# Optimization experiments

Hardware: AMD Instinct MI355X
Metric: run time of the kernel (lower is better)

The kernel has to match this reference:

```python
import jax, jax.numpy as jnp
import numpy as np

B, S, D, H = 4, 2048, 512, 8
DH = D // H


def setup_inputs() -> dict:
    key = jax.random.key(0)
    ks = jax.random.split(key, 6)
    embeddings = jax.random.normal(ks[0], (B, S, D), dtype=jnp.float32)
    token_masks = jax.random.randint(ks[1], (B, S), 0, 2, dtype=jnp.int32)
    # keras 'random_normal' initializer: stddev 0.05
    Wq = 0.05 * jax.random.normal(ks[2], (D, D), dtype=jnp.float32)
    Wk = 0.05 * jax.random.normal(ks[3], (D, D), dtype=jnp.float32)
    Wv = 0.05 * jax.random.normal(ks[4], (D, D), dtype=jnp.float32)
    Wo = 0.05 * jax.random.normal(ks[5], (D, D), dtype=jnp.float32)
    return {"embeddings": embeddings, "token_masks": token_masks,
            "Wq": Wq, "Wk": Wk, "Wv": Wv, "Wo": Wo}


def reference(embeddings, token_masks, Wq, Wk, Wv, Wo):
    b, s, d = embeddings.shape
    h, dh = H, d // H
    # QKV projections -> (b, h, s, dh)
    def split_heads(x):
        return x.reshape(b, s, h, dh).transpose(0, 2, 1, 3)
    Q = split_heads(embeddings @ Wq)
    K = split_heads(embeddings @ Wk)
    V = split_heads(embeddings @ Wv)
    scores = jnp.einsum('bhqd,bhkd->bhqk', Q, K) / jnp.sqrt(jnp.float32(dh))
    # causal (lower-triangular) mask combined with padding mask on both q and k
    causal = jnp.tril(jnp.ones((s, s), dtype=jnp.float32))
    tm = token_masks.astype(jnp.float32)
    attn_mask = causal[None, None, :, :] * tm[:, None, None, :] * tm[:, None, :, None]
    scores = jnp.where(attn_mask > 0, scores, jnp.float32(-1e30))
    weights = jax.nn.softmax(scores, axis=-1)  # dropout omitted (inference/eval mode)
    context = jnp.einsum('bhqk,bhkd->bhqd', weights, V)
    context = context.transpose(0, 2, 1, 3).reshape(b, s, d)
    return context @ Wo
```

## Files before the change

kernel.cpp:

```cpp
#include <hip/hip_runtime.h>
#include <hip/hip_bf16.h>
#include <stdint.h>

#define BATCH 4
#define SEQ 2048
#define DMODEL 512
#define NHEAD 8
#define HD 64

#define C1 0.18033688f
#define BIAS2 -23.0831207f

using f32x4 = __attribute__((ext_vector_type(4))) float;
using bfrag = __attribute__((ext_vector_type(8))) short;

__device__ __forceinline__ short f2bf(float f) {
  uint32_t x = __builtin_bit_cast(uint32_t, f);
  uint32_t r = (x + 0x7fffu + ((x >> 16) & 1u)) >> 16;
  return (short)r;
}
__device__ __forceinline__ short f2bf_fast(float f) {
  return (short)((__builtin_bit_cast(uint32_t, f) + 0x8000u) >> 16);
}
__device__ __forceinline__ float bf2f(short s) {
  return __builtin_bit_cast(float, ((uint32_t)(uint16_t)s) << 16);
}
__device__ __forceinline__ void gl_lds16(const void* g, void* l) {
  __builtin_amdgcn_global_load_lds(
      (const __attribute__((address_space(1))) void*)g,
      (__attribute__((address_space(3))) void*)l, 16, 0, 0);
}
__device__ __forceinline__ bool sniff_f32(const void* p, int tid) {
  const uint32_t* xw = (const uint32_t*)p;
  const int lane = tid & 63;
  const uint32_t w1 = xw[lane], w2 = xw[64 + lane];
  bool bad = (((w1 >> 7) & 0xffu) >= 0xB0u) | (((w1 >> 23) & 0xffu) >= 0xB0u) |
             (((w2 >> 7) & 0xffu) >= 0xB0u) | (((w2 >> 23) & 0xffu) >= 0xB0u);
  return __ballot(bad) != 0ull;
}

__global__ __launch_bounds__(256) void prep(const void* __restrict__ X,
                                            const void* __restrict__ w0,
                                            const void* __restrict__ w1,
                                            const void* __restrict__ w2,
                                            const void* __restrict__ w3,
                                            short* __restrict__ Xb,
                                            short* __restrict__ wtAll,
                                            float* __restrict__ mv) {
  const int blk = blockIdx.x, tid = threadIdx.x;
  if (blk < 2048) {
    const bool isf32 = sniff_f32(X, tid);
    const int i = (blk * 256 + tid) * 8;
    if (isf32) {
      const float* f = (const float*)X;
      short r[8];
#pragma unroll
      for (int j = 0; j < 8; ++j) r[j] = f2bf(f[i + j]);
      *(bfrag*)&Xb[i] = *(bfrag*)r;
    } else {
      *(bfrag*)&Xb[i] = *(const bfrag*)&((const short*)X)[i];
    }
  } else if (blk < 3072) {
    __shared__ short t[32][33];
    const int idx = blk - 2048;
    const int z = idx >> 8, rem = idx & 255;
    const void* in = (z == 0) ? w0 : (z == 1) ? w1 : (z == 2) ? w2 : w3;
    short* out = wtAll + (size_t)z * DMODEL * DMODEL;
    const int tx = tid & 31, ty = tid >> 5;
    const bool isf32 = sniff_f32(in, tid);
    const int n0 = (rem & 15) * 32, k0 = (rem >> 4) * 32;
#pragma unroll
    for (int i = ty; i < 32; i += 8) {
      const int idx2 = (k0 + i) * DMODEL + n0 + tx;
      t[i][tx] = isf32 ? f2bf(((const float*)in)[idx2]) : ((const short*)in)[idx2];
    }
    __syncthreads();
#pragma unroll
    for (int i = ty; i < 32; i += 8) out[(n0 + i) * DMODEL + k0 + tx] = t[tx][i];
  } else {
#pragma unroll
    for (int j = 0; j < 8; ++j) mv[tid * 8 + j] = 0.f;
  }
}

__global__ __launch_bounds__(256) void gemm_qkv(const short* __restrict__ X,
                                                const short* __restrict__ WtAll,
                                                short* __restrict__ Qo,
                                                short* __restrict__ Ko,
                                                short* __restrict__ Vo,
                                                float* __restrict__ mv) {
  __shared__ __align__(16) short As[2][128 * 32];
  __shared__ __align__(16) short Bs[2][128 * 32];
  const int which = blockIdx.z;
  const short* Wt = WtAll + which * DMODEL * DMODEL;
  const int m0 = blockIdx.y * 128, n0 = blockIdx.x * 128;
  const int tid = threadIdx.x, lane = tid & 63, wave = tid >> 6;
  const int l15 = lane & 15, quad = lane >> 4;
  const int wm = wave >> 1, wn = wave & 1;
  const int lrow = lane >> 2, lcol = (lane & 3) * 8;
  f32x4 acc[4][4] = {};
  auto stage = [&](int kc, int bb) {
#pragma unroll
    for (int i = 0; i < 2; ++i) {
      const int r0 = (wave * 2 + i) * 16;
      gl_lds16(&X[(size_t)(m0 + r0 + lrow) * DMODEL + kc + lcol], &As[bb][r0 * 32]);
      gl_lds16(&Wt[(size_t)(n0 + r0 + lrow) * DMODEL + kc + lcol], &Bs[bb][r0 * 32]);
    }
  };
  stage(0, 0);
  __syncthreads();
  int bb = 0;
  for (int kc = 0; kc < DMODEL; kc += 32) {
    if (kc + 32 < DMODEL) stage(kc + 32, bb ^ 1);
    bfrag a[4], b[4];
#pragma unroll
    for (int t = 0; t < 4; ++t) {
      a[t] = *(const bfrag*)&As[bb][(wm * 64 + t * 16 + l15) * 32 + quad * 8];
      b[t] = *(const bfrag*)&Bs[bb][(wn * 64 + t * 16 + l15) * 32 + quad * 8];
    }
#pragma unroll
    for (int tm = 0; tm < 4; ++tm)
#pragma unroll
      for (int tn = 0; tn < 4; ++tn)
        acc[tm][tn] = __builtin_amdgcn_mfma_f32_16x16x32_bf16(a[tm], b[tn], acc[tm][tn], 0, 0, 0);
    __syncthreads();
    bb ^= 1;
  }
  short* O = (which == 0) ? Qo : (which == 1) ? Ko : Vo;
#pragma unroll
  for (int tn = 0; tn < 4; ++tn) {
    const int col = n0 + wn * 64 + tn * 16 + l15;
    const int h = col >> 6, d = col & 63;
#pragma unroll
    for (int tm = 0; tm < 4; ++tm) {
#pragma unroll
      for (int r = 0; r < 4; ++r) {
        const int row = m0 + wm * 64 + tm * 16 + quad * 4 + r;
        const int b = row >> 11, s = row & 2047;
        O[((b * NHEAD + h) * SEQ + s) * HD + d] = f2bf(acc[tm][tn][r]);
      }
    }
  }
  if (which == 2) {
    const int b = (m0 + wm * 64) >> 11;
#pragma unroll
    for (int tn = 0; tn < 4; ++tn) {
      float s = 0.f;
#pragma unroll
      for (int tm = 0; tm < 4; ++tm)
#pragma unroll
        for (int r = 0; r < 4; ++r) s += acc[tm][tn][r];
      s += __shfl_xor(s, 16);
      s += __shfl_xor(s, 32);
      if (quad == 0) {
        const int col = n0 + wn * 64 + tn * 16 + l15;
        const int h = col >> 6, d = col & 63;
        atomicAdd(&mv[(b * NHEAD + h) * 64 + d], s);
      }
    }
  }
}

__global__ __launch_bounds__(256) void gemm_out(const short* __restrict__ X,
                                                const short* __restrict__ Wt,
                                                float* __restrict__ O) {
  __shared__ __align__(16) short As[2][128 * 32];
  __shared__ __align__(16) short Bs[2][128 * 32];
  const int m0 = blockIdx.y * 128, n0 = blockIdx.x * 128;
  const int tid = threadIdx.x, lane = tid & 63, wave = tid >> 6;
  const int l15 = lane & 15, quad = lane >> 4;
  const int wm = wave >> 1, wn = wave & 1;
  const int lrow = lane >> 2, lcol = (lane & 3) * 8;
  f32x4 acc[4][4] = {};
  auto stage = [&](int kc, int bb) {
#pragma unroll
    for (int i = 0; i < 2; ++i) {
      const int r0 = (wave * 2 + i) * 16;
      gl_lds16(&X[(size_t)(m0 + r0 + lrow) * DMODEL + kc + lcol], &As[bb][r0 * 32]);
      gl_lds16(&Wt[(size_t)(n0 + r0 + lrow) * DMODEL + kc + lcol], &Bs[bb][r0 * 32]);
    }
  };
  stage(0, 0);
  __syncthreads();
  int bb = 0;
  for (int kc = 0; kc < DMODEL; kc += 32) {
    if (kc + 32 < DMODEL) stage(kc + 32, bb ^ 1);
    bfrag a[4], b[4];
#pragma unroll
    for (int t = 0; t < 4; ++t) {
      a[t] = *(const bfrag*)&As[bb][(wm * 64 + t * 16 + l15) * 32 + quad * 8];
      b[t] = *(const bfrag*)&Bs[bb][(wn * 64 + t * 16 + l15) * 32 + quad * 8];
    }
#pragma unroll
    for (int tm = 0; tm < 4; ++tm)
#pragma unroll
      for (int tn = 0; tn < 4; ++tn)
        acc[tm][tn] = __builtin_amdgcn_mfma_f32_16x16x32_bf16(a[tm], b[tn], acc[tm][tn], 0, 0, 0);
    __syncthreads();
    bb ^= 1;
  }
#pragma unroll
  for (int tm = 0; tm < 4; ++tm)
#pragma unroll
    for (int tn = 0; tn < 4; ++tn) {
      const int col = n0 + wn * 64 + tn * 16 + l15;
#pragma unroll
      for (int r = 0; r < 4; ++r) {
        const int row = m0 + wm * 64 + tm * 16 + quad * 4 + r;
        O[(size_t)row * DMODEL + col] = acc[tm][tn][r];
      }
    }
}

__global__ __launch_bounds__(256, 4) void attn(const short* __restrict__ Q,
                                               const short* __restrict__ K,
                                               const short* __restrict__ V,
                                               const int* __restrict__ tmask,
                                               const float* __restrict__ meanV,
                                               short* __restrict__ ctx) {
  __shared__ __align__(16) short Ks[64 * 72];
  __shared__ __align__(16) short Vts[64 * 64];
  __shared__ __align__(16) short Ps[4 * 16 * 64];
  __shared__ int tmq[64];
  __shared__ int tmk[64];
  const int m2 = blockIdx.x >> 3, a3 = blockIdx.x & 7;
  const int j2 = blockIdx.y >> 3, b3 = blockIdx.y & 7;
  const int quart = (m2 + j2) & 3;
  const int qi = quart * 8 + ((quart & 1) ? (7 - a3) : a3);
  const int bh = j2 * 8 + b3;
  const int b = bh >> 3, h = bh & 7;
  const int q0 = qi * 64;
  const int tid = threadIdx.x, lane = tid & 63, wave = tid >> 6;
  const int l15 = lane & 15, quad = lane >> 4;
  const size_t base = (size_t)bh * SEQ * HD;

  bfrag qa0 = *(const bfrag*)&Q[base + (size_t)(q0 + wave * 16 + l15) * HD + quad * 8];
  bfrag qa1 = *(const bfrag*)&Q[base + (size_t)(q0 + wave * 16 + l15) * HD + 32 + quad * 8];
  if (tid < 64) tmq[tid] = tmask[b * SEQ + q0 + tid];

  f32x4 accO[4] = {};
  float lrow[4] = {0.f, 0.f, 0.f, 0.f};

  const int rp = tid >> 3, sgp = tid & 7;
  bfrag kA, kB, vA, vB;
  int tmreg = 0;

  auto prefetch = [&](int kc) {
    const size_t o0 = base + (size_t)(kc + 2 * rp) * HD + sgp * 8;
    kA = *(const bfrag*)&K[o0];
    kB = *(const bfrag*)&K[o0 + HD];
    vA = *(const bfrag*)&V[o0];
    vB = *(const bfrag*)&V[o0 + HD];
    if (tid < 64) tmreg = tmask[b * SEQ + kc + tid];
  };
  auto store_lds = [&]() {
    *(bfrag*)&Ks[(2 * rp) * 72 + sgp * 8] = kA;
    *(bfrag*)&Ks[(2 * rp + 1) * 72 + sgp * 8] = kB;
    const int g = ((rp >> 2) ^ ((sgp & 1) << 2) ^ (sgp >> 1)) & 7;
    const int kpos = (2 * rp) & 7;
#pragma unroll
    for (int j = 0; j < 8; ++j) {
      const uint32_t w = (uint32_t)(uint16_t)vA[j] | ((uint32_t)(uint16_t)vB[j] << 16);
      *(uint32_t*)&Vts[(sgp * 8 + j) * 64 + g * 8 + kpos] = w;
    }
    if (tid < 64) tmk[tid] = tmreg;
  };
  auto compute = [&](bool diag) {
    f32x4 sacc[4] = {};
#pragma unroll
    for (int t = 0; t < 4; ++t) {
      bfrag b0 = *(const bfrag*)&Ks[(t * 16 + l15) * 72 + quad * 8];
      sacc[t] = __builtin_amdgcn_mfma_f32_16x16x32_bf16(qa0, b0, sacc[t], 0, 0, 0);
    }
#pragma unroll
    for (int t = 0; t < 4; ++t) {
      bfrag b1 = *(const bfrag*)&Ks[(t * 16 + l15) * 72 + 32 + quad * 8];
      sacc[t] = __builtin_amdgcn_mfma_f32_16x16x32_bf16(qa1, b1, sacc[t], 0, 0, 0);
    }
    float badd[4];
#pragma unroll
    for (int t = 0; t < 4; ++t) badd[t] = tmk[t * 16 + l15] ? BIAS2 : -1e30f;
#pragma unroll
    for (int r = 0; r < 4; ++r) {
      const int m = quad * 4 + r;
#pragma unroll
      for (int t = 0; t < 4; ++t) {
        float p = exp2f(fmaf(sacc[t][r], C1, badd[t]));
        if (diag && (t * 16 + l15 > wave * 16 + m)) p = 0.f;
        lrow[r] += p;
        const int g = ((t * 2 + (l15 >> 3)) ^ (m & 7) ^ ((m >> 3) << 1)) & 7;
        Ps[wave * 1024 + m * 64 + g * 8 + (l15 & 7)] = f2bf_fast(p);
      }
    }
#pragma unroll
    for (int ks = 0; ks < 2; ++ks) {
#pragma unroll
      for (int t = 0; t < 4; ++t) {
        const int gp = ((ks * 4 + quad) ^ (l15 & 7) ^ ((l15 >> 3) << 1)) & 7;
        bfrag pa = *(const bfrag*)&Ps[wave * 1024 + l15 * 64 + gp * 8];
        const int d = t * 16 + l15;
        const int gv = ((ks * 4 + quad) ^ ((l15 >> 3) << 2) ^ t) & 7;
        bfrag vb = *(const bfrag*)&Vts[d * 64 + gv * 8];
        accO[t] = __builtin_amdgcn_mfma_f32_16x16x32_bf16(pa, vb, accO[t], 0, 0, 0);
      }
    }
  };

  prefetch(0);
  for (int kc = 0; kc <= q0; kc += 64) {
    __syncthreads();
    store_lds();
    __syncthreads();
    if (kc < q0) prefetch(kc + 64);
    compute(kc == q0);
  }

#pragma unroll
  for (int r = 0; r < 4; ++r) {
    float l = lrow[r];
    l += __shfl_xor(l, 1);
    l += __shfl_xor(l, 2);
    l += __shfl_xor(l, 4);
    l += __shfl_xor(l, 8);
    lrow[r] = 1.f / l;
  }
  const int qrow_loc = wave * 16 + quad * 4;
#pragma unroll
  for (int t = 0; t < 4; ++t) {
    const int d = t * 16 + l15;
    const float mvd = meanV[bh * 64 + d] * (1.f / 2048.f);
#pragma unroll
    for (int r = 0; r < 4; ++r) {
      const int row = qrow_loc + r;
      float val = accO[t][r] * lrow[r];
      if (tmq[row] == 0) val = mvd;
      ctx[((size_t)(b * SEQ + q0 + row)) * DMODEL + h * HD + d] = f2bf(val);
    }
  }
}

extern "C" void kernel_launch(void* const* d_in, const int* in_sizes, int n_in,
                              void* d_out, int out_size, void* d_ws, size_t ws_size,
                              hipStream_t stream) {
  const void* X = d_in[0];
  const int* tmask = (const int*)d_in[1];
  const void* Wq = d_in[2];
  const void* Wk = d_in[3];
  const void* Wv = d_in[4];
  const void* Wo = d_in[5];
  float* out = (float*)d_out;
  char* ws = (char*)d_ws;

  const size_t WELEM = (size_t)DMODEL * DMODEL;
  const size_t TELEM = (size_t)BATCH * NHEAD * SEQ * HD;

  float* mv = (float*)(ws + 4096);
  short* wt = (short*)(ws + 4096 + 8192);
  short* Xb = (short*)(ws + 4096 + 8192 + 2097152);
  short* Qb = Xb + TELEM;
  short* Kb = Qb + TELEM;
  short* Vb = Kb + TELEM;
  short* Cb = Vb + TELEM;

  prep<<<3073, 256, 0, stream>>>(X, Wq, Wk, Wv, Wo, Xb, wt, mv);
  gemm_qkv<<<dim3(4, 64, 3), 256, 0, stream>>>(Xb, wt, Qb, Kb, Vb, mv);
  attn<<<dim3(32, 32), 256, 0, stream>>>(Qb, Kb, Vb, tmask, mv, Cb);
  gemm_out<<<dim3(4, 64), 256, 0, stream>>>(Cb, wt + 3 * WELEM, out);
}
```

Measured before the change: 163.9 us.

## Use two waves per attention block, each handling 32 query rows

The attention block shrinks from four to two waves, and each wave now processes two 16-row query tiles. Every K and V fragment read from LDS therefore feeds two MFMAs, and the cooperative K/V load covers four rows per thread instead of two. This raises register pressure and halves the threads per block, which could lower latency hiding and occupancy. The launch bounds are changed to match.

Result: slower. 228.8 us (+39.6%).

```diff
diff --git a/kernel.cpp b/kernel.cpp
--- a/kernel.cpp
+++ b/kernel.cpp
@@ -212,7 +212,7 @@
     }
 }
 
-__global__ __launch_bounds__(256, 4) void attn(const short* __restrict__ Q,
+__global__ __launch_bounds__(128, 3) void attn(const short* __restrict__ Q,
                                                const short* __restrict__ K,
                                                const short* __restrict__ V,
                                                const int* __restrict__ tmask,
@@ -220,7 +220,7 @@
                                                short* __restrict__ ctx) {
   __shared__ __align__(16) short Ks[64 * 72];
   __shared__ __align__(16) short Vts[64 * 64];
-  __shared__ __align__(16) short Ps[4 * 16 * 64];
+  __shared__ __align__(16) short Ps[2 * 32 * 64];
   __shared__ int tmq[64];
   __shared__ int tmk[64];
   const int m2 = blockIdx.x >> 3, a3 = blockIdx.x & 7;
@@ -234,48 +234,62 @@
   const int l15 = lane & 15, quad = lane >> 4;
   const size_t base = (size_t)bh * SEQ * HD;
 
-  bfrag qa0 = *(const bfrag*)&Q[base + (size_t)(q0 + wave * 16 + l15) * HD + quad * 8];
-  bfrag qa1 = *(const bfrag*)&Q[base + (size_t)(q0 + wave * 16 + l15) * HD + 32 + quad * 8];
+  const size_t qr0 = base + (size_t)(q0 + wave * 16 + l15) * HD;
+  const size_t qr1 = qr0 + (size_t)32 * HD;
+  bfrag q00 = *(const bfrag*)&Q[qr0 + quad * 8];
+  bfrag q01 = *(const bfrag*)&Q[qr0 + 32 + quad * 8];
+  bfrag q10 = *(const bfrag*)&Q[qr1 + quad * 8];
+  bfrag q11 = *(const bfrag*)&Q[qr1 + 32 + quad * 8];
   if (tid < 64) tmq[tid] = tmask[b * SEQ + q0 + tid];
 
-  f32x4 accO[4] = {};
-  float lrow[4] = {0.f, 0.f, 0.f, 0.f};
+  f32x4 accO0[4] = {}, accO1[4] = {};
+  float lr0[4] = {0.f, 0.f, 0.f, 0.f}, lr1[4] = {0.f, 0.f, 0.f, 0.f};
 
   const int rp = tid >> 3, sgp = tid & 7;
-  bfrag kA, kB, vA, vB;
+  bfrag kA, kB, kC, kD, vA, vB, vC, vD;
   int tmreg = 0;
 
   auto prefetch = [&](int kc) {
-    const size_t o0 = base + (size_t)(kc + 2 * rp) * HD + sgp * 8;
+    const size_t o0 = base + (size_t)(kc + 4 * rp) * HD + sgp * 8;
     kA = *(const bfrag*)&K[o0];
     kB = *(const bfrag*)&K[o0 + HD];
+    kC = *(const bfrag*)&K[o0 + 2 * HD];
+    kD = *(const bfrag*)&K[o0 + 3 * HD];
     vA = *(const bfrag*)&V[o0];
     vB = *(const bfrag*)&V[o0 + HD];
+    vC = *(const bfrag*)&V[o0 + 2 * HD];
+    vD = *(const bfrag*)&V[o0 + 3 * HD];
     if (tid < 64) tmreg = tmask[b * SEQ + kc + tid];
   };
   auto store_lds = [&]() {
-    *(bfrag*)&Ks[(2 * rp) * 72 + sgp * 8] = kA;
-    *(bfrag*)&Ks[(2 * rp + 1) * 72 + sgp * 8] = kB;
-    const int g = ((rp >> 2) ^ ((sgp & 1) << 2) ^ (sgp >> 1)) & 7;
-    const int kpos = (2 * rp) & 7;
-#pragma unroll
-    for (int j = 0; j < 8; ++j) {
-      const uint32_t w = (uint32_t)(uint16_t)vA[j] | ((uint32_t)(uint16_t)vB[j] << 16);
-      *(uint32_t*)&Vts[(sgp * 8 + j) * 64 + g * 8 + kpos] = w;
+    *(bfrag*)&Ks[(4 * rp + 0) * 72 + sgp * 8] = kA;
+    *(bfrag*)&Ks[(4 * rp + 1) * 72 + sgp * 8] = kB;
+    *(bfrag*)&Ks[(4 * rp + 2) * 72 + sgp * 8] = kC;
+    *(bfrag*)&Ks[(4 * rp + 3) * 72 + sgp * 8] = kD;
+#pragma unroll
+    for (int p = 0; p < 2; ++p) {
+      const int k0 = 4 * rp + 2 * p;
+      const int g = ((k0 >> 3) ^ ((sgp & 1) << 2) ^ (sgp >> 1)) & 7;
+      const int kpos = k0 & 7;
+      const bfrag vLo = p ? vC : vA, vHi = p ? vD : vB;
+#pragma unroll
+      for (int j = 0; j < 8; ++j) {
+        const uint32_t w = (uint32_t)(uint16_t)vLo[j] | ((uint32_t)(uint16_t)vHi[j] << 16);
+        *(uint32_t*)&Vts[(sgp * 8 + j) * 64 + g * 8 + kpos] = w;
+      }
     }
     if (tid < 64) tmk[tid] = tmreg;
   };
   auto compute = [&](bool diag) {
-    f32x4 sacc[4] = {};
+    f32x4 sa[4] = {}, sb[4] = {};
 #pragma unroll
     for (int t = 0; t < 4; ++t) {
       bfrag b0 = *(const bfrag*)&Ks[(t * 16 + l15) * 72 + quad * 8];
-      sacc[t] = __builtin_amdgcn_mfma_f32_16x16x32_bf16(qa0, b0, sacc[t], 0, 0, 0);
-    }
-#pragma unroll
-    for (int t = 0; t < 4; ++t) {
+      sa[t] = __builtin_amdgcn_mfma_f32_16x16x32_bf16(q00, b0, sa[t], 0, 0, 0);
+      sb[t] = __builtin_amdgcn_mfma_f32_16x16x32_bf16(q10, b0, sb[t], 0, 0, 0);
       bfrag b1 = *(const bfrag*)&Ks[(t * 16 + l15) * 72 + 32 + quad * 8];
-      sacc[t] = __builtin_amdgcn_mfma_f32_16x16x32_bf16(qa1, b1, sacc[t], 0, 0, 0);
+      sa[t] = __builtin_amdgcn_mfma_f32_16x16x32_bf16(q01, b1, sa[t], 0, 0, 0);
+      sb[t] = __builtin_amdgcn_mfma_f32_16x16x32_bf16(q11, b1, sb[t], 0, 0, 0);
     }
     float badd[4];
 #pragma unroll
@@ -285,23 +299,38 @@
       const int m = quad * 4 + r;
 #pragma unroll
       for (int t = 0; t < 4; ++t) {
-        float p = exp2f(fmaf(sacc[t][r], C1, badd[t]));
+        float p = exp2f(fmaf(sa[t][r], C1, badd[t]));
         if (diag && (t * 16 + l15 > wave * 16 + m)) p = 0.f;
-        lrow[r] += p;
+        lr0[r] += p;
         const int g = ((t * 2 + (l15 >> 3)) ^ (m & 7) ^ ((m >> 3) << 1)) & 7;
-        Ps[wave * 1024 + m * 64 + g * 8 + (l15 & 7)] = f2bf_fast(p);
+        Ps[wave * 2048 + m * 64 + g * 8 + (l15 & 7)] = f2bf_fast(p);
+      }
+    }
+#pragma unroll
+    for (int r = 0; r < 4; ++r) {
+      const int m = quad * 4 + r;
+#pragma unroll
+      for (int t = 0; t < 4; ++t) {
+        float p = exp2f(fmaf(sb[t][r], C1, badd[t]));
+        if (diag && (t * 16 + l15 > 32 + wave * 16 + m)) p = 0.f;
+        lr1[r] += p;
+        const int g = ((t * 2 + (l15 >> 3)) ^ (m & 7) ^ (((m >> 3) << 1) ^ 4)) & 7;
+        Ps[wave * 2048 + (16 + m) * 64 + g * 8 + (l15 & 7)] = f2bf_fast(p);
       }
     }
 #pragma unroll
     for (int ks = 0; ks < 2; ++ks) {
+      const int gp0 = ((ks * 4 + quad) ^ (l15 & 7) ^ ((l15 >> 3) << 1)) & 7;
+      const int gp1 = gp0 ^ 4;
+      bfrag pa0 = *(const bfrag*)&Ps[wave * 2048 + l15 * 64 + gp0 * 8];
+      bfrag pa1 = *(const bfrag*)&Ps[wave * 2048 + (16 + l15) * 64 + gp1 * 8];
 #pragma unroll
       for (int t = 0; t < 4; ++t) {
-        const int gp = ((ks * 4 + quad) ^ (l15 & 7) ^ ((l15 >> 3) << 1)) & 7;
-        bfrag pa = *(const bfrag*)&Ps[wave * 1024 + l15 * 64 + gp * 8];
         const int d = t * 16 + l15;
         const int gv = ((ks * 4 + quad) ^ ((l15 >> 3) << 2) ^ t) & 7;
         bfrag vb = *(const bfrag*)&Vts[d * 64 + gv * 8];
-        accO[t] = __builtin_amdgcn_mfma_f32_16x16x32_bf16(pa, vb, accO[t], 0, 0, 0);
+        accO0[t] = __builtin_amdgcn_mfma_f32_16x16x32_bf16(pa0, vb, accO0[t], 0, 0, 0);
+        accO1[t] = __builtin_amdgcn_mfma_f32_16x16x32_bf16(pa1, vb, accO1[t], 0, 0, 0);
       }
     }
   };
@@ -317,24 +346,34 @@
 
 #pragma unroll
   for (int r = 0; r < 4; ++r) {
-    float l = lrow[r];
+    float l = lr0[r];
     l += __shfl_xor(l, 1);
     l += __shfl_xor(l, 2);
     l += __shfl_xor(l, 4);
     l += __shfl_xor(l, 8);
-    lrow[r] = 1.f / l;
-  }
-  const int qrow_loc = wave * 16 + quad * 4;
+    lr0[r] = 1.f / l;
+    float l2 = lr1[r];
+    l2 += __shfl_xor(l2, 1);
+    l2 += __shfl_xor(l2, 2);
+    l2 += __shfl_xor(l2, 4);
+    l2 += __shfl_xor(l2, 8);
+    lr1[r] = 1.f / l2;
+  }
+  const int qrl = wave * 16 + quad * 4;
 #pragma unroll
   for (int t = 0; t < 4; ++t) {
     const int d = t * 16 + l15;
     const float mvd = meanV[bh * 64 + d] * (1.f / 2048.f);
 #pragma unroll
     for (int r = 0; r < 4; ++r) {
-      const int row = qrow_loc + r;
-      float val = accO[t][r] * lrow[r];
-      if (tmq[row] == 0) val = mvd;
-      ctx[((size_t)(b * SEQ + q0 + row)) * DMODEL + h * HD + d] = f2bf(val);
+      const int row0 = qrl + r;
+      float v0 = accO0[t][r] * lr0[r];
+      if (tmq[row0] == 0) v0 = mvd;
+      ctx[((size_t)(b * SEQ + q0 + row0)) * DMODEL + h * HD + d] = f2bf(v0);
+      const int row1 = 32 + qrl + r;
+      float v1 = accO1[t][r] * lr1[r];
+      if (tmq[row1] == 0) v1 = mvd;
+      ctx[((size_t)(b * SEQ + q0 + row1)) * DMODEL + h * HD + d] = f2bf(v1);
     }
   }
 }
@@ -364,6 +403,6 @@
 
   prep<<<3073, 256, 0, stream>>>(X, Wq, Wk, Wv, Wo, Xb, wt, mv);
   gemm_qkv<<<dim3(4, 64, 3), 256, 0, stream>>>(Xb, wt, Qb, Kb, Vb, mv);
-  attn<<<dim3(32, 32), 256, 0, stream>>>(Qb, Kb, Vb, tmask, mv, Cb);
+  attn<<<dim3(32, 32), 128, 0, stream>>>(Qb, Kb, Vb, tmask, mv, Cb);
   gemm_out<<<dim3(4, 64), 256, 0, stream>>>(Cb, wt + 3 * WELEM, out);
 }
```
